# Kernel optimization log

Hardware: AMD Instinct MI355X
Metric: run time of the kernel (lower is better)

Reference implementation:

```python
import jax, jax.numpy as jnp
import numpy as np

NUM_FIELDS = 10
VOCAB = 100000
EMBED_DIM = 8
BATCH = 16384

def setup_inputs() -> dict:
    key = jax.random.key(0)
    k1, k2, k3 = jax.random.split(key, 3)
    x = jax.random.randint(k1, (BATCH, NUM_FIELDS), 0, VOCAB)  # categorical ids per field
    # field-aware embedding tables: V[i, j, v, :] = embedding of feature v in field i
    # used when interacting with field j  (xavier-ish small init)
    V = jax.random.normal(k2, (NUM_FIELDS, NUM_FIELDS, VOCAB, EMBED_DIM), dtype=jnp.float32) * 0.01
    # linear (first-order) weights, one scalar per feature id per field
    L = jax.random.normal(k3, (NUM_FIELDS, VOCAB), dtype=jnp.float32) * 0.01
    bias = jnp.zeros((), dtype=jnp.float32)
    return {"x": x, "bias": bias, "L": L, "V": V}

def reference(x, bias, L, V):
    B, F = x.shape
    idx = jnp.arange(F)
    xt = x.T  # (F, B)
    # first-order term: sum_i L[i, x[:, i]] -> (B,)
    first = L[idx[:, None], xt].sum(axis=0)
    # field-aware gather: E[i, j, b, :] = V[i, j, x[b, i], :]  -> (F, F, B, D)
    E = V[idx[:, None, None], idx[None, :, None], xt[:, None, :]]
    # pairwise interactions: P[i, j, b] = <V[i][j](x_i), V[j][i](x_j)>
    P = jnp.einsum('ijbd,jibd->ijb', E, E)
    mask = jnp.triu(jnp.ones((F, F), dtype=bool), k=1)  # i < j only
    second = jnp.where(mask[:, :, None], P, 0.0).sum(axis=(0, 1))  # (B,)
    logit = bias + first + second
    return jax.nn.sigmoid(logit)[:, None]  # (B, 1)
```

## Files before the change

kernel.cpp:

```cpp
#include <hip/hip_runtime.h>
#include <math.h>

#define NFIELDS 10
#define VOCAB   100000
#define EDIM    8
#define BATCH   16384
#define NPAIR   45


__global__ __launch_bounds__(256) void ffm_first(
    const int*   __restrict__ x,
    const float* __restrict__ bias,
    const float* __restrict__ L,
    float*       __restrict__ out)
{
    const int b = blockIdx.x * 256 + threadIdx.x;
    float acc = bias[0];
    #pragma unroll
    for (int i = 0; i < NFIELDS; ++i) {
        const int xi = x[b * NFIELDS + i];
        acc += L[(size_t)i * VOCAB + (size_t)xi];
    }
    out[b] = acc;
}

__global__ __launch_bounds__(256) void ffm_pairs(
    const int*   __restrict__ x,
    const float* __restrict__ V,
    float*       __restrict__ out)
{
    const int pb = blockIdx.x;
    const int p  = pb >> 6;
    const int b  = ((pb & 63) << 8) + threadIdx.x;

    int i = 0, q = p, cnt = NFIELDS - 1;
    while (q >= cnt) { q -= cnt; ++i; --cnt; }
    const int j = i + 1 + q;

    const int xi = x[b * NFIELDS + i];
    const int xj = x[b * NFIELDS + j];

    const float* va = V + (((size_t)i * NFIELDS + j) * VOCAB + (size_t)xi) * EDIM;
    const float* vb = V + (((size_t)j * NFIELDS + i) * VOCAB + (size_t)xj) * EDIM;

    const float4 a0 = ((const float4*)va)[0];
    const float4 a1 = ((const float4*)va)[1];
    const float4 b0 = ((const float4*)vb)[0];
    const float4 b1 = ((const float4*)vb)[1];

    const float dot = a0.x * b0.x + a0.y * b0.y + a0.z * b0.z + a0.w * b0.w
                    + a1.x * b1.x + a1.y * b1.y + a1.z * b1.z + a1.w * b1.w;

    atomicAdd(&out[b], dot);
}

__global__ __launch_bounds__(256) void ffm_sigmoid(
    float* __restrict__ out)
{
    const int b = blockIdx.x * 256 + threadIdx.x;
    const float logit = out[b];
    out[b] = 1.0f / (1.0f + expf(-logit));
}

extern "C" void kernel_launch(void* const* d_in, const int* in_sizes, int n_in,
                              void* d_out, int out_size, void* d_ws, size_t ws_size,
                              hipStream_t stream) {
    const int*   x    = (const int*)  d_in[0];
    const float* bias = (const float*)d_in[1];
    const float* L    = (const float*)d_in[2];
    const float* V    = (const float*)d_in[3];
    float*       out  = (float*)d_out;

    ffm_first<<<BATCH / 256, 256, 0, stream>>>(x, bias, L, out);

    ffm_pairs<<<NPAIR * 64, 256, 0, stream>>>(x, V, out);

    ffm_sigmoid<<<BATCH / 256, 256, 0, stream>>>(out);
}
```

Baseline: 396.8 us.

## Fuse first-order, pairwise and sigmoid into one wave-per-row kernel

Replaces three kernels (first-order sum, per-pair atomic accumulation, sigmoid) with a single kernel where each 64-lane wavefront handles one batch row: 45 lanes compute pair dot products, 10 lanes fetch linear weights, and a shuffle reduction produces the logit before the sigmoid. This removes the global atomics, the extra launches and the intermediate round trips through the output buffer. It also switches address math to 32-bit unsigned offsets. Nine of the 64 lanes sit idle, and per-row gather locality changes.

```diff
diff --git a/kernel.cpp b/kernel.cpp
--- a/kernel.cpp
+++ b/kernel.cpp
@@ -7,59 +7,57 @@
 #define BATCH   16384
 #define NPAIR   45
 
-
-__global__ __launch_bounds__(256) void ffm_first(
+__global__ __launch_bounds__(256) void ffm_kernel(
     const int*   __restrict__ x,
     const float* __restrict__ bias,
     const float* __restrict__ L,
-    float*       __restrict__ out)
-{
-    const int b = blockIdx.x * 256 + threadIdx.x;
-    float acc = bias[0];
-    #pragma unroll
-    for (int i = 0; i < NFIELDS; ++i) {
-        const int xi = x[b * NFIELDS + i];
-        acc += L[(size_t)i * VOCAB + (size_t)xi];
-    }
-    out[b] = acc;
-}
-
-__global__ __launch_bounds__(256) void ffm_pairs(
-    const int*   __restrict__ x,
     const float* __restrict__ V,
     float*       __restrict__ out)
 {
-    const int pb = blockIdx.x;
-    const int p  = pb >> 6;
-    const int b  = ((pb & 63) << 8) + threadIdx.x;
+    const int lane = threadIdx.x & 63;
+    const int wave = threadIdx.x >> 6;
+    const int b    = blockIdx.x * 4 + wave;
 
-    int i = 0, q = p, cnt = NFIELDS - 1;
-    while (q >= cnt) { q -= cnt; ++i; --cnt; }
-    const int j = i + 1 + q;
+    float acc = 0.0f;
 
-    const int xi = x[b * NFIELDS + i];
-    const int xj = x[b * NFIELDS + j];
+    if (lane < NPAIR) {
+        int p = lane;
+        int i = 0;
+        int cnt = NFIELDS - 1;
+        while (p >= cnt) { p -= cnt; ++i; --cnt; }
+        const int j = i + 1 + p;
 
-    const float* va = V + (((size_t)i * NFIELDS + j) * VOCAB + (size_t)xi) * EDIM;
-    const float* vb = V + (((size_t)j * NFIELDS + i) * VOCAB + (size_t)xj) * EDIM;
+        const int xi = x[b * NFIELDS + i];
+        const int xj = x[b * NFIELDS + j];
 
-    const float4 a0 = ((const float4*)va)[0];
-    const float4 a1 = ((const float4*)va)[1];
-    const float4 b0 = ((const float4*)vb)[0];
-    const float4 b1 = ((const float4*)vb)[1];
+        const unsigned oa = ((unsigned)(i * NFIELDS + j) * (unsigned)VOCAB
+                             + (unsigned)xi) * (unsigned)(EDIM * 4);
+        const unsigned ob = ((unsigned)(j * NFIELDS + i) * (unsigned)VOCAB
+                             + (unsigned)xj) * (unsigned)(EDIM * 4);
+        const float4* va = (const float4*)((const char*)V + oa);
+        const float4* vb = (const float4*)((const char*)V + ob);
 
-    const float dot = a0.x * b0.x + a0.y * b0.y + a0.z * b0.z + a0.w * b0.w
-                    + a1.x * b1.x + a1.y * b1.y + a1.z * b1.z + a1.w * b1.w;
+        const float4 a0 = va[0];
+        const float4 a1 = va[1];
+        const float4 b0 = vb[0];
+        const float4 b1 = vb[1];
 
-    atomicAdd(&out[b], dot);
-}
+        acc = a0.x * b0.x + a0.y * b0.y + a0.z * b0.z + a0.w * b0.w
+            + a1.x * b1.x + a1.y * b1.y + a1.z * b1.z + a1.w * b1.w;
+    } else if (lane < NPAIR + NFIELDS) {
+        const int i  = lane - NPAIR;
+        const int xi = x[b * NFIELDS + i];
+        acc = L[(unsigned)i * (unsigned)VOCAB + (unsigned)xi];
+    }
 
-__global__ __launch_bounds__(256) void ffm_sigmoid(
-    float* __restrict__ out)
-{
-    const int b = blockIdx.x * 256 + threadIdx.x;
-    const float logit = out[b];
-    out[b] = 1.0f / (1.0f + expf(-logit));
+    #pragma unroll
+    for (int off = 32; off > 0; off >>= 1)
+        acc += __shfl_down(acc, off, 64);
+
+    if (lane == 0) {
+        const float logit = acc + bias[0];
+        out[b] = 1.0f / (1.0f + expf(-logit));
+    }
 }
 
 extern "C" void kernel_launch(void* const* d_in, const int* in_sizes, int n_in,
@@ -71,9 +69,6 @@
     const float* V    = (const float*)d_in[3];
     float*       out  = (float*)d_out;
 
-    ffm_first<<<BATCH / 256, 256, 0, stream>>>(x, bias, L, out);
-
-    ffm_pairs<<<NPAIR * 64, 256, 0, stream>>>(x, V, out);
-
-    ffm_sigmoid<<<BATCH / 256, 256, 0, stream>>>(out);
+    const int blocks = BATCH / 4;
+    ffm_kernel<<<blocks, 256, 0, stream>>>(x, bias, L, V, out);
 }
```

Measured after the change: 390.8 us. No clear change (-1.5%).
